# Optimization experiments

Hardware: AMD Instinct MI355X
Metric: run time of the kernel (lower is better)

The kernel has to match this reference:

```python
import jax, jax.numpy as jnp
import numpy as np

# Module hyperparameters (init_kwargs)
D = 2          # input_dim
OUT = 3        # output_dim
T = 14         # log2 hash table size
L = 16         # number of levels
F = 2          # features per level
N_MIN, N_MAX = 16, 512
B = 1048576    # batch of query points
HIDDEN = 64

_b = np.exp((np.log(N_MAX) - np.log(N_MIN)) / (L - 1))
RES = jnp.asarray(np.floor(N_MIN * _b ** np.arange(L)).astype(np.float32))  # [L]

# voxel corner offsets [D, 2^D] (same construction as torch module)
_border = np.empty((D, 2 ** D), dtype=np.int32)
for _i in range(D):
    _border[_i, :] = np.array(([0] * 2 ** _i + [1] * 2 ** _i) * 2 ** (D - _i - 1), dtype=np.int32)
BORDER = jnp.asarray(_border)

# NVIDIA tiny-cuda-nn primes; uint32 arithmetic is exact for the low T bits
# (low 14 bits of a product/xor only depend on low 32 bits), matching torch's
# int64 multiply-xor followed by mod 2^T.
PRIMES = jnp.array([1, 2654435761, 805459861, 3674653429, 2097192037, 1434869437, 2165219737][:D], dtype=jnp.uint32)


def setup_inputs() -> dict:
    key = jax.random.key(0)
    ks = jax.random.split(key, 8)
    x = jax.random.uniform(ks[0], (B, D), jnp.float32)  # coords in [0,1)
    tables = jax.random.uniform(ks[1], (L, 2 ** T, F), jnp.float32, -1e-4, 1e-4)
    W1 = jax.random.normal(ks[2], (HIDDEN, L * F), jnp.float32) * 0.05
    b1 = jnp.zeros((HIDDEN,), jnp.float32)
    W2 = jax.random.normal(ks[3], (HIDDEN, HIDDEN), jnp.float32) * 0.05
    b2 = jnp.zeros((HIDDEN,), jnp.float32)
    W3 = jax.random.normal(ks[4], (OUT, HIDDEN), jnp.float32) * 0.05
    b3 = jnp.zeros((OUT,), jnp.float32)
    return {"x": x, "tables": tables, "W1": W1, "b1": b1, "W2": W2, "b2": b2, "W3": W3, "b3": b3}


def reference(x, tables, W1, b1, W2, b2, W3, b3):
    n = x.shape[0]
    # scale coords by each level resolution: [B, D, L]
    scaled = x[:, :, None] * RES[None, None, :]
    grid = jnp.floor(scaled).astype(jnp.int32)                     # [B, D, L]
    corners = grid[..., None] + BORDER[None, :, None, :]           # [B, D, L, 2^D]
    # spatial hash: xor of coord * prime per dimension, mod 2^T
    h = jnp.zeros((n, L, 2 ** D), jnp.uint32)
    for i in range(D):
        h = h ^ (corners[:, i].astype(jnp.uint32) * PRIMES[i])
    idx = (h & jnp.uint32(2 ** T - 1)).astype(jnp.int32)           # [B, L, 2^D]
    # per-level embedding gather: [B, L, 2^D, F]
    looked = tables[jnp.arange(L)[None, :, None], idx]
    # (bi/tri)linear interpolation weights: prod over dims -> [B, L, 2^D]
    w = jnp.prod(1.0 - jnp.abs(scaled[..., None] - corners.astype(x.dtype)), axis=1)
    feat = jnp.einsum('blc,blcf->blf', w, looked).reshape(n, L * F)  # [B, L*F]
    # small MLP head
    h1 = jax.nn.relu(feat @ W1.T + b1)
    h2 = jax.nn.relu(h1 @ W2.T + b2)
    return h2 @ W3.T + b3
```

## Files before the change

kernel.cpp:

```cpp
#include <hip/hip_runtime.h>
#include <hip/hip_bf16.h>
#include <math.h>


#define TBL_MASK 16383u
#define PRIME1   2654435761u

typedef __attribute__((ext_vector_type(8))) short short8;
typedef __attribute__((ext_vector_type(4))) float f32x4;
typedef __attribute__((ext_vector_type(4))) unsigned int uint4v;

struct ResArr { float r[16]; };

#define WS_W1H 0
#define WS_W1L 2048
#define WS_W2H 4096
#define WS_W2L 8192
#define WS_W3H 12288
#define WS_W3L 13312

__device__ __forceinline__ unsigned short bf16rn(float f) {
    __hip_bfloat16 h = __float2bfloat16(f);
    return __builtin_bit_cast(unsigned short, h);
}
__device__ __forceinline__ float bf16tof(unsigned short u) {
    unsigned int x = ((unsigned int)u) << 16;
    return __builtin_bit_cast(float, x);
}
__device__ __forceinline__ short8 ldFrag(const unsigned short* p) {
    return __builtin_bit_cast(short8, *(const uint4v*)p);
}

#define MFMA(a, b, c) __builtin_amdgcn_mfma_f32_16x16x32_bf16((a), (b), (c), 0, 0, 0)

__global__ __launch_bounds__(256) void prep_weights(
    const float* __restrict__ W1,
    const float* __restrict__ W2,
    const float* __restrict__ W3,
    unsigned short* __restrict__ ws)
{
    const int t = blockIdx.x * 256 + threadIdx.x;
    if (t < 2048) {
        const float v = W1[t];
        const unsigned short hb = bf16rn(v);
        ws[WS_W1H + t] = hb;
        ws[WS_W1L + t] = bf16rn(v - bf16tof(hb));
    } else if (t < 2048 + 4096) {
        const int i = t - 2048;
        const float v = W2[i];
        const unsigned short hb = bf16rn(v);
        ws[WS_W2H + i] = hb;
        ws[WS_W2L + i] = bf16rn(v - bf16tof(hb));
    } else if (t < 2048 + 4096 + 1024) {
        const int i = t - 6144;
        const int r = i >> 6, c = i & 63;
        const float v = (r < 3) ? W3[r * 64 + c] : 0.0f;
        const unsigned short hb = bf16rn(v);
        ws[WS_W3H + i] = hb;
        ws[WS_W3L + i] = bf16rn(v - bf16tof(hb));
    }
}

__global__ __launch_bounds__(64) void mh_mfma(
    const float* __restrict__ x,
    const float* __restrict__ tables,
    const float* __restrict__ b1,
    const float* __restrict__ b2,
    const float* __restrict__ b3,
    const unsigned short* __restrict__ ws,
    float* __restrict__ out,
    ResArr res, int n)
{
    __shared__ char smem[10240];
    unsigned short* sF  = (unsigned short*)smem;
    unsigned short* sAH = (unsigned short*)smem;
    unsigned short* sAL = (unsigned short*)(smem + 4608);

    const int L  = threadIdx.x;
    const int ln = L & 15;
    const int q  = L >> 4;
    const long base = (long)blockIdx.x * 64;
    long s = base + L;
    if (s >= (long)n) s = (long)n - 1;

    const float2 xv = reinterpret_cast<const float2*>(x)[s];
    const float2* __restrict__ tbl2 = reinterpret_cast<const float2*>(tables);

    #pragma unroll 8
    for (int l = 0; l < 16; ++l) {
        const float r  = res.r[l];
        const float sx = xv.x * r;
        const float sy = xv.y * r;
        const float gx = floorf(sx);
        const float gy = floorf(sy);
        const unsigned ux = (unsigned)(int)gx;
        const unsigned uy = (unsigned)(int)gy;
        const unsigned hy0 = uy * PRIME1;
        const unsigned hy1 = hy0 + PRIME1;
        const unsigned i00 = ( ux       ^ hy0) & TBL_MASK;
        const unsigned i10 = ((ux + 1u) ^ hy0) & TBL_MASK;
        const unsigned i01 = ( ux       ^ hy1) & TBL_MASK;
        const unsigned i11 = ((ux + 1u) ^ hy1) & TBL_MASK;
        const float2* tl = tbl2 + (l << 14);
        const float2 t00 = tl[i00];
        const float2 t10 = tl[i10];
        const float2 t01 = tl[i01];
        const float2 t11 = tl[i11];
        const float wx0 = 1.0f - fabsf(sx - gx);
        const float wx1 = 1.0f - fabsf(sx - (gx + 1.0f));
        const float wy0 = 1.0f - fabsf(sy - gy);
        const float wy1 = 1.0f - fabsf(sy - (gy + 1.0f));
        const float w00 = wx0 * wy0;
        const float w10 = wx1 * wy0;
        const float w01 = wx0 * wy1;
        const float w11 = wx1 * wy1;
        const float f0 = fmaf(w00, t00.x, fmaf(w10, t10.x, fmaf(w01, t01.x, w11 * t11.x)));
        const float f1 = fmaf(w00, t00.y, fmaf(w10, t10.y, fmaf(w01, t01.y, w11 * t11.y)));
        const unsigned short h0 = bf16rn(f0);
        const unsigned short h1e = bf16rn(f1);
        const unsigned short l0 = bf16rn(f0 - bf16tof(h0));
        const unsigned short l1 = bf16rn(f1 - bf16tof(h1e));
        *(unsigned int*)&sF[L * 40 + 2 * l]        = (unsigned)h0 | ((unsigned)h1e << 16);
        *(unsigned int*)&sF[2560 + L * 40 + 2 * l] = (unsigned)l0 | ((unsigned)l1 << 16);
    }

    short8 fah[2][2], fal[2][2];
    #pragma unroll
    for (int mh = 0; mh < 2; ++mh)
        #pragma unroll
        for (int mt = 0; mt < 2; ++mt) {
            const int row = mh * 32 + mt * 16 + ln;
            fah[mh][mt] = ldFrag(&sF[row * 40 + q * 8]);
            fal[mh][mt] = ldFrag(&sF[2560 + row * 40 + q * 8]);
        }

    float b1v[4], b2v[4];
    #pragma unroll
    for (int nt = 0; nt < 4; ++nt) { b1v[nt] = b1[nt * 16 + ln]; b2v[nt] = b2[nt * 16 + ln]; }
    const float b3v = (ln < 3) ? b3[ln] : 0.0f;

    const f32x4 zero4 = {0.0f, 0.0f, 0.0f, 0.0f};

    for (int mh = 0; mh < 2; ++mh) {
        f32x4 acc1[2][4];
        #pragma unroll
        for (int mt = 0; mt < 2; ++mt)
            #pragma unroll
            for (int nt = 0; nt < 4; ++nt) acc1[mt][nt] = zero4;

        #pragma unroll
        for (int nt = 0; nt < 4; ++nt) {
            const int off = (nt * 16 + ln) * 32 + q * 8;
            const short8 bh = ldFrag(ws + WS_W1H + off);
            const short8 bl = ldFrag(ws + WS_W1L + off);
            #pragma unroll
            for (int mt = 0; mt < 2; ++mt) {
                f32x4 a = acc1[mt][nt];
                a = MFMA(fal[mh][mt], bh, a);
                a = MFMA(fah[mh][mt], bl, a);
                a = MFMA(fah[mh][mt], bh, a);
                acc1[mt][nt] = a;
            }
        }
        #pragma unroll
        for (int mt = 0; mt < 2; ++mt)
            #pragma unroll
            for (int nt = 0; nt < 4; ++nt) {
                const int col = nt * 16 + ln;
                #pragma unroll
                for (int r = 0; r < 4; ++r) {
                    float v = fmaxf(acc1[mt][nt][r] + b1v[nt], 0.0f);
                    const unsigned short hb = bf16rn(v);
                    const unsigned short lb = bf16rn(v - bf16tof(hb));
                    const int rl = mt * 16 + q * 4 + r;
                    sAH[rl * 72 + col] = hb;
                    sAL[rl * 72 + col] = lb;
                }
            }

        short8 a2h[2][2], a2l[2][2];
        #pragma unroll
        for (int mt = 0; mt < 2; ++mt)
            #pragma unroll
            for (int ks = 0; ks < 2; ++ks) {
                const int row = mt * 16 + ln;
                a2h[mt][ks] = ldFrag(&sAH[row * 72 + ks * 32 + q * 8]);
                a2l[mt][ks] = ldFrag(&sAL[row * 72 + ks * 32 + q * 8]);
            }
        f32x4 acc2[2][4];
        #pragma unroll
        for (int mt = 0; mt < 2; ++mt)
            #pragma unroll
            for (int nt = 0; nt < 4; ++nt) acc2[mt][nt] = zero4;

        #pragma unroll
        for (int nt = 0; nt < 4; ++nt)
            #pragma unroll
            for (int ks = 0; ks < 2; ++ks) {
                const int off = (nt * 16 + ln) * 64 + ks * 32 + q * 8;
                const short8 bh = ldFrag(ws + WS_W2H + off);
                const short8 bl = ldFrag(ws + WS_W2L + off);
                #pragma unroll
                for (int mt = 0; mt < 2; ++mt) {
                    f32x4 a = acc2[mt][nt];
                    a = MFMA(a2l[mt][ks], bh, a);
                    a = MFMA(a2h[mt][ks], bl, a);
                    a = MFMA(a2h[mt][ks], bh, a);
                    acc2[mt][nt] = a;
                }
            }
        #pragma unroll
        for (int mt = 0; mt < 2; ++mt)
            #pragma unroll
            for (int nt = 0; nt < 4; ++nt) {
                const int col = nt * 16 + ln;
                #pragma unroll
                for (int r = 0; r < 4; ++r) {
                    float v = fmaxf(acc2[mt][nt][r] + b2v[nt], 0.0f);
                    const unsigned short hb = bf16rn(v);
                    const unsigned short lb = bf16rn(v - bf16tof(hb));
                    const int rl = mt * 16 + q * 4 + r;
                    sAH[rl * 72 + col] = hb;
                    sAL[rl * 72 + col] = lb;
                }
            }

        short8 a3h[2][2], a3l[2][2];
        #pragma unroll
        for (int mt = 0; mt < 2; ++mt)
            #pragma unroll
            for (int ks = 0; ks < 2; ++ks) {
                const int row = mt * 16 + ln;
                a3h[mt][ks] = ldFrag(&sAH[row * 72 + ks * 32 + q * 8]);
                a3l[mt][ks] = ldFrag(&sAL[row * 72 + ks * 32 + q * 8]);
            }
        f32x4 acc3[2] = {zero4, zero4};
        #pragma unroll
        for (int ks = 0; ks < 2; ++ks) {
            const int off = ln * 64 + ks * 32 + q * 8;
            const short8 bh = ldFrag(ws + WS_W3H + off);
            const short8 bl = ldFrag(ws + WS_W3L + off);
            #pragma unroll
            for (int mt = 0; mt < 2; ++mt) {
                f32x4 a = acc3[mt];
                a = MFMA(a3l[mt][ks], bh, a);
                a = MFMA(a3h[mt][ks], bl, a);
                a = MFMA(a3h[mt][ks], bh, a);
                acc3[mt] = a;
            }
        }
        if (ln < 3) {
            #pragma unroll
            for (int mt = 0; mt < 2; ++mt)
                #pragma unroll
                for (int r = 0; r < 4; ++r) {
                    const long sg = base + mh * 32 + mt * 16 + q * 4 + r;
                    if (sg < (long)n) out[sg * 3 + ln] = acc3[mt][r] + b3v;
                }
        }
    }
}

extern "C" void kernel_launch(void* const* d_in, const int* in_sizes, int n_in,
                              void* d_out, int out_size, void* d_ws, size_t ws_size,
                              hipStream_t stream) {
    const float* x      = (const float*)d_in[0];
    const float* tables = (const float*)d_in[1];
    const float* W1     = (const float*)d_in[2];
    const float* b1v    = (const float*)d_in[3];
    const float* W2     = (const float*)d_in[4];
    const float* b2v    = (const float*)d_in[5];
    const float* W3     = (const float*)d_in[6];
    const float* b3v    = (const float*)d_in[7];
    float* out = (float*)d_out;
    unsigned short* ws = (unsigned short*)d_ws;

    const int n = in_sizes[0] / 2;

    ResArr ra;
    const double bb = exp((log(512.0) - log(16.0)) / 15.0);
    for (int k = 0; k < 16; ++k) ra.r[k] = (float)floor(16.0 * pow(bb, (double)k));

    hipLaunchKernelGGL(prep_weights, dim3(28), dim3(256), 0, stream, W1, W2, W3, ws);
    hipLaunchKernelGGL(mh_mfma, dim3((n + 63) / 64), dim3(64), 0, stream,
                       x, tables, b1v, b2v, b3v, ws, out, ra, n);
}
```

Measured before the change: 255.7 us.

## Double-buffer hash encoding across multiple sample groups per block

Each single-wave block now handles eight 64-sample groups instead of one. The hash-grid encoding of the next group is written into a second LDS buffer while the MLP MFMAs run on the current group, so gather latency can overlap with matrix work. The grid shrinks eightfold and explicit lgkmcnt waits are added around LDS reuse. The risks are lower parallelism, since there are far fewer waves for latency hiding on a gather-bound kernel, and the extra LDS footprint.

```diff
diff --git a/kernel.cpp b/kernel.cpp
--- a/kernel.cpp
+++ b/kernel.cpp
@@ -5,6 +5,8 @@
 
 #define TBL_MASK 16383u
 #define PRIME1   2654435761u
+#define G_PER    8
+#define LDS_DRAIN() asm volatile("s_waitcnt lgkmcnt(0)" ::: "memory")
 
 typedef __attribute__((ext_vector_type(8))) short short8;
 typedef __attribute__((ext_vector_type(4))) float f32x4;
@@ -61,32 +63,15 @@
     }
 }
 
-__global__ __launch_bounds__(64) void mh_mfma(
-    const float* __restrict__ x,
-    const float* __restrict__ tables,
-    const float* __restrict__ b1,
-    const float* __restrict__ b2,
-    const float* __restrict__ b3,
-    const unsigned short* __restrict__ ws,
-    float* __restrict__ out,
-    ResArr res, int n)
+__device__ __forceinline__ void encode_group(
+    const float* __restrict__ x, const float2* __restrict__ tbl2,
+    const ResArr& res, long sBase, int L, int n,
+    unsigned short* __restrict__ dH, unsigned short* __restrict__ dL)
 {
-    __shared__ char smem[10240];
-    unsigned short* sF  = (unsigned short*)smem;
-    unsigned short* sAH = (unsigned short*)smem;
-    unsigned short* sAL = (unsigned short*)(smem + 4608);
-
-    const int L  = threadIdx.x;
-    const int ln = L & 15;
-    const int q  = L >> 4;
-    const long base = (long)blockIdx.x * 64;
-    long s = base + L;
+    long s = sBase + L;
     if (s >= (long)n) s = (long)n - 1;
-
     const float2 xv = reinterpret_cast<const float2*>(x)[s];
-    const float2* __restrict__ tbl2 = reinterpret_cast<const float2*>(tables);
-
-    #pragma unroll 8
+    #pragma unroll 4
     for (int l = 0; l < 16; ++l) {
         const float r  = res.r[l];
         const float sx = xv.x * r;
@@ -120,19 +105,29 @@
         const unsigned short h1e = bf16rn(f1);
         const unsigned short l0 = bf16rn(f0 - bf16tof(h0));
         const unsigned short l1 = bf16rn(f1 - bf16tof(h1e));
-        *(unsigned int*)&sF[L * 40 + 2 * l]        = (unsigned)h0 | ((unsigned)h1e << 16);
-        *(unsigned int*)&sF[2560 + L * 40 + 2 * l] = (unsigned)l0 | ((unsigned)l1 << 16);
+        *(unsigned int*)&dH[L * 40 + 2 * l] = (unsigned)h0 | ((unsigned)h1e << 16);
+        *(unsigned int*)&dL[L * 40 + 2 * l] = (unsigned)l0 | ((unsigned)l1 << 16);
     }
-
-    short8 fah[2][2], fal[2][2];
-    #pragma unroll
-    for (int mh = 0; mh < 2; ++mh)
-        #pragma unroll
-        for (int mt = 0; mt < 2; ++mt) {
-            const int row = mh * 32 + mt * 16 + ln;
-            fah[mh][mt] = ldFrag(&sF[row * 40 + q * 8]);
-            fal[mh][mt] = ldFrag(&sF[2560 + row * 40 + q * 8]);
-        }
+}
+
+__global__ __launch_bounds__(64) void mh_mfma(
+    const float* __restrict__ x,
+    const float* __restrict__ tables,
+    const float* __restrict__ b1,
+    const float* __restrict__ b2,
+    const float* __restrict__ b3,
+    const unsigned short* __restrict__ ws,
+    float* __restrict__ out,
+    ResArr res, int n)
+{
+    __shared__ __align__(16) unsigned short smem[2 * 5120];
+
+    const int L  = threadIdx.x;
+    const int ln = L & 15;
+    const int q  = L >> 4;
+    const long blockBase = (long)blockIdx.x * (64 * G_PER);
+
+    const float2* __restrict__ tbl2 = reinterpret_cast<const float2*>(tables);
 
     float b1v[4], b2v[4];
     #pragma unroll
@@ -141,122 +136,152 @@
 
     const f32x4 zero4 = {0.0f, 0.0f, 0.0f, 0.0f};
 
-    for (int mh = 0; mh < 2; ++mh) {
-        f32x4 acc1[2][4];
+    encode_group(x, tbl2, res, blockBase, L, n, smem, smem + 2560);
+
+    #pragma unroll 1
+    for (int g = 0; g < G_PER; ++g) {
+        const int cb = g & 1;
+        unsigned short* bufC = smem + cb * 5120;
+        unsigned short* bufN = smem + (cb ^ 1) * 5120;
+        const long gBase = blockBase + (long)g * 64;
+
+        LDS_DRAIN();
+
+        short8 fah[2][2], fal[2][2];
         #pragma unroll
-        for (int mt = 0; mt < 2; ++mt)
-            #pragma unroll
-            for (int nt = 0; nt < 4; ++nt) acc1[mt][nt] = zero4;
-
-        #pragma unroll
-        for (int nt = 0; nt < 4; ++nt) {
-            const int off = (nt * 16 + ln) * 32 + q * 8;
-            const short8 bh = ldFrag(ws + WS_W1H + off);
-            const short8 bl = ldFrag(ws + WS_W1L + off);
+        for (int mh = 0; mh < 2; ++mh)
             #pragma unroll
             for (int mt = 0; mt < 2; ++mt) {
-                f32x4 a = acc1[mt][nt];
-                a = MFMA(fal[mh][mt], bh, a);
-                a = MFMA(fah[mh][mt], bl, a);
-                a = MFMA(fah[mh][mt], bh, a);
-                acc1[mt][nt] = a;
+                const int row = mh * 32 + mt * 16 + ln;
+                fah[mh][mt] = ldFrag(&bufC[row * 40 + q * 8]);
+                fal[mh][mt] = ldFrag(&bufC[2560 + row * 40 + q * 8]);
             }
-        }
-        #pragma unroll
-        for (int mt = 0; mt < 2; ++mt)
+        LDS_DRAIN();
+
+        if (g + 1 < G_PER)
+            encode_group(x, tbl2, res, blockBase + (long)(g + 1) * 64, L, n,
+                         bufN, bufN + 2560);
+
+        unsigned short* sAH = bufC;
+        unsigned short* sAL = bufC + 2304;
+
+        for (int mh = 0; mh < 2; ++mh) {
+            f32x4 acc1[2][4];
+            #pragma unroll
+            for (int mt = 0; mt < 2; ++mt)
+                #pragma unroll
+                for (int nt = 0; nt < 4; ++nt) acc1[mt][nt] = zero4;
             #pragma unroll
             for (int nt = 0; nt < 4; ++nt) {
-                const int col = nt * 16 + ln;
-                #pragma unroll
-                for (int r = 0; r < 4; ++r) {
-                    float v = fmaxf(acc1[mt][nt][r] + b1v[nt], 0.0f);
-                    const unsigned short hb = bf16rn(v);
-                    const unsigned short lb = bf16rn(v - bf16tof(hb));
-                    const int rl = mt * 16 + q * 4 + r;
-                    sAH[rl * 72 + col] = hb;
-                    sAL[rl * 72 + col] = lb;
+                const int off = (nt * 16 + ln) * 32 + q * 8;
+                const short8 bh = ldFrag(ws + WS_W1H + off);
+                const short8 bl = ldFrag(ws + WS_W1L + off);
+                #pragma unroll
+                for (int mt = 0; mt < 2; ++mt) {
+                    f32x4 a = acc1[mt][nt];
+                    a = MFMA(fal[mh][mt], bh, a);
+                    a = MFMA(fah[mh][mt], bl, a);
+                    a = MFMA(fah[mh][mt], bh, a);
+                    acc1[mt][nt] = a;
                 }
             }
-
-        short8 a2h[2][2], a2l[2][2];
-        #pragma unroll
-        for (int mt = 0; mt < 2; ++mt)
+            #pragma unroll
+            for (int mt = 0; mt < 2; ++mt)
+                #pragma unroll
+                for (int nt = 0; nt < 4; ++nt) {
+                    const int col = nt * 16 + ln;
+                    #pragma unroll
+                    for (int r = 0; r < 4; ++r) {
+                        const float v = fmaxf(acc1[mt][nt][r] + b1v[nt], 0.0f);
+                        const unsigned short hb = bf16rn(v);
+                        const int rl = mt * 16 + q * 4 + r;
+                        sAH[rl * 72 + col] = hb;
+                        sAL[rl * 72 + col] = bf16rn(v - bf16tof(hb));
+                    }
+                }
+            LDS_DRAIN();
+
+            short8 a2h[2][2], a2l[2][2];
+            #pragma unroll
+            for (int mt = 0; mt < 2; ++mt)
+                #pragma unroll
+                for (int ks = 0; ks < 2; ++ks) {
+                    const int row = mt * 16 + ln;
+                    a2h[mt][ks] = ldFrag(&sAH[row * 72 + ks * 32 + q * 8]);
+                    a2l[mt][ks] = ldFrag(&sAL[row * 72 + ks * 32 + q * 8]);
+                }
+            LDS_DRAIN();
+            f32x4 acc2[2][4];
+            #pragma unroll
+            for (int mt = 0; mt < 2; ++mt)
+                #pragma unroll
+                for (int nt = 0; nt < 4; ++nt) acc2[mt][nt] = zero4;
+            #pragma unroll
+            for (int nt = 0; nt < 4; ++nt)
+                #pragma unroll
+                for (int ks = 0; ks < 2; ++ks) {
+                    const int off = (nt * 16 + ln) * 64 + ks * 32 + q * 8;
+                    const short8 bh = ldFrag(ws + WS_W2H + off);
+                    const short8 bl = ldFrag(ws + WS_W2L + off);
+                    #pragma unroll
+                    for (int mt = 0; mt < 2; ++mt) {
+                        f32x4 a = acc2[mt][nt];
+                        a = MFMA(a2l[mt][ks], bh, a);
+                        a = MFMA(a2h[mt][ks], bl, a);
+                        a = MFMA(a2h[mt][ks], bh, a);
+                        acc2[mt][nt] = a;
+                    }
+                }
+            #pragma unroll
+            for (int mt = 0; mt < 2; ++mt)
+                #pragma unroll
+                for (int nt = 0; nt < 4; ++nt) {
+                    const int col = nt * 16 + ln;
+                    #pragma unroll
+                    for (int r = 0; r < 4; ++r) {
+                        const float v = fmaxf(acc2[mt][nt][r] + b2v[nt], 0.0f);
+                        const unsigned short hb = bf16rn(v);
+                        const int rl = mt * 16 + q * 4 + r;
+                        sAH[rl * 72 + col] = hb;
+                        sAL[rl * 72 + col] = bf16rn(v - bf16tof(hb));
+                    }
+                }
+            LDS_DRAIN();
+
+            short8 a3h[2][2], a3l[2][2];
+            #pragma unroll
+            for (int mt = 0; mt < 2; ++mt)
+                #pragma unroll
+                for (int ks = 0; ks < 2; ++ks) {
+                    const int row = mt * 16 + ln;
+                    a3h[mt][ks] = ldFrag(&sAH[row * 72 + ks * 32 + q * 8]);
+                    a3l[mt][ks] = ldFrag(&sAL[row * 72 + ks * 32 + q * 8]);
+                }
+            LDS_DRAIN();
+            f32x4 acc3[2] = {zero4, zero4};
             #pragma unroll
             for (int ks = 0; ks < 2; ++ks) {
-                const int row = mt * 16 + ln;
-                a2h[mt][ks] = ldFrag(&sAH[row * 72 + ks * 32 + q * 8]);
-                a2l[mt][ks] = ldFrag(&sAL[row * 72 + ks * 32 + q * 8]);
+                const int off = ln * 64 + ks * 32 + q * 8;
+                const short8 bh = ldFrag(ws + WS_W3H + off);
+                const short8 bl = ldFrag(ws + WS_W3L + off);
+                #pragma unroll
+                for (int mt = 0; mt < 2; ++mt) {
+                    f32x4 a = acc3[mt];
+                    a = MFMA(a3l[mt][ks], bh, a);
+                    a = MFMA(a3h[mt][ks], bl, a);
+                    a = MFMA(a3h[mt][ks], bh, a);
+                    acc3[mt] = a;
+                }
             }
-        f32x4 acc2[2][4];
-        #pragma unroll
-        for (int mt = 0; mt < 2; ++mt)
-            #pragma unroll
-            for (int nt = 0; nt < 4; ++nt) acc2[mt][nt] = zero4;
-
-        #pragma unroll
-        for (int nt = 0; nt < 4; ++nt)
-            #pragma unroll
-            for (int ks = 0; ks < 2; ++ks) {
-                const int off = (nt * 16 + ln) * 64 + ks * 32 + q * 8;
-                const short8 bh = ldFrag(ws + WS_W2H + off);
-                const short8 bl = ldFrag(ws + WS_W2L + off);
-                #pragma unroll
-                for (int mt = 0; mt < 2; ++mt) {
-                    f32x4 a = acc2[mt][nt];
-                    a = MFMA(a2l[mt][ks], bh, a);
-                    a = MFMA(a2h[mt][ks], bl, a);
-                    a = MFMA(a2h[mt][ks], bh, a);
-                    acc2[mt][nt] = a;
-                }
+            if (ln < 3) {
+                #pragma unroll
+                for (int mt = 0; mt < 2; ++mt)
+                    #pragma unroll
+                    for (int r = 0; r < 4; ++r) {
+                        const long sg = gBase + mh * 32 + mt * 16 + q * 4 + r;
+                        if (sg < (long)n) out[sg * 3 + ln] = acc3[mt][r] + b3v;
+                    }
             }
-        #pragma unroll
-        for (int mt = 0; mt < 2; ++mt)
-            #pragma unroll
-            for (int nt = 0; nt < 4; ++nt) {
-                const int col = nt * 16 + ln;
-                #pragma unroll
-                for (int r = 0; r < 4; ++r) {
-                    float v = fmaxf(acc2[mt][nt][r] + b2v[nt], 0.0f);
-                    const unsigned short hb = bf16rn(v);
-                    const unsigned short lb = bf16rn(v - bf16tof(hb));
-                    const int rl = mt * 16 + q * 4 + r;
-                    sAH[rl * 72 + col] = hb;
-                    sAL[rl * 72 + col] = lb;
-                }
-            }
-
-        short8 a3h[2][2], a3l[2][2];
-        #pragma unroll
-        for (int mt = 0; mt < 2; ++mt)
-            #pragma unroll
-            for (int ks = 0; ks < 2; ++ks) {
-                const int row = mt * 16 + ln;
-                a3h[mt][ks] = ldFrag(&sAH[row * 72 + ks * 32 + q * 8]);
-                a3l[mt][ks] = ldFrag(&sAL[row * 72 + ks * 32 + q * 8]);
-            }
-        f32x4 acc3[2] = {zero4, zero4};
-        #pragma unroll
-        for (int ks = 0; ks < 2; ++ks) {
-            const int off = ln * 64 + ks * 32 + q * 8;
-            const short8 bh = ldFrag(ws + WS_W3H + off);
-            const short8 bl = ldFrag(ws + WS_W3L + off);
-            #pragma unroll
-            for (int mt = 0; mt < 2; ++mt) {
-                f32x4 a = acc3[mt];
-                a = MFMA(a3l[mt][ks], bh, a);
-                a = MFMA(a3h[mt][ks], bl, a);
-                a = MFMA(a3h[mt][ks], bh, a);
-                acc3[mt] = a;
-            }
-        }
-        if (ln < 3) {
-            #pragma unroll
-            for (int mt = 0; mt < 2; ++mt)
-                #pragma unroll
-                for (int r = 0; r < 4; ++r) {
-                    const long sg = base + mh * 32 + mt * 16 + q * 4 + r;
-                    if (sg < (long)n) out[sg * 3 + ln] = acc3[mt][r] + b3v;
-                }
         }
     }
 }
@@ -282,6 +307,7 @@
     for (int k = 0; k < 16; ++k) ra.r[k] = (float)floor(16.0 * pow(bb, (double)k));
 
     hipLaunchKernelGGL(prep_weights, dim3(28), dim3(256), 0, stream, W1, W2, W3, ws);
-    hipLaunchKernelGGL(mh_mfma, dim3((n + 63) / 64), dim3(64), 0, stream,
+    const int spb = 64 * G_PER;
+    hipLaunchKernelGGL(mh_mfma, dim3((n + spb - 1) / spb), dim3(64), 0, stream,
                        x, tables, b1v, b2v, b3v, ws, out, ra, n);
 }
```

Result: slower. 279.4 us (+9.3%).
